# Optimization experiments

Measured on AMD Instinct MI355X. Metric: run time of the kernel, lower is better.

Reference implementation:

```python
import jax, jax.numpy as jnp
import numpy as np

N, E, H, NIN, DD = 10000, 160000, 128, 128, 256
SCALE = 30.0
EPS = 1e-5

def _ln(x, g, b):
    mu = jnp.mean(x, axis=-1, keepdims=True)
    var = jnp.mean((x - mu) ** 2, axis=-1, keepdims=True)
    return (x - mu) * jax.lax.rsqrt(var + EPS) * g + b

def _gelu(x):
    return jax.nn.gelu(x, approximate=False)  # torch nn.GELU default (erf)

def setup_inputs() -> dict:
    key = jax.random.key(0)
    ks = jax.random.split(key, 16)
    def w(k, i, o):
        return jax.random.normal(k, (i, o), jnp.float32) * (1.0 / np.sqrt(i))
    return {
        "h_V": jax.random.normal(ks[0], (N, H), jnp.float32),
        "h_E": jax.random.normal(ks[1], (E, H + NIN), jnp.float32),
        "edge_idx": jax.random.randint(ks[2], (2, E), 0, N, jnp.int32),
        # message MLP: (H+NIN)->H, H->H
        "m_w0": w(ks[3], H + NIN, H), "m_b0": jnp.zeros((H,), jnp.float32),
        "m_w1": w(ks[4], H, H),       "m_b1": jnp.zeros((H,), jnp.float32),
        # dense MLP: H->DD, DD->DD, final DD->H
        "d_w0": w(ks[5], H, DD),  "d_b0": jnp.zeros((DD,), jnp.float32),
        "d_w1": w(ks[6], DD, DD), "d_b1": jnp.zeros((DD,), jnp.float32),
        "d_w2": w(ks[7], DD, H),  "d_b2": jnp.zeros((H,), jnp.float32),
        # LayerNorm params
        "g1": jnp.ones((H,), jnp.float32), "be1": jnp.zeros((H,), jnp.float32),
        "g2": jnp.ones((H,), jnp.float32), "be2": jnp.zeros((H,), jnp.float32),
    }

def reference(h_V, h_E, edge_idx, m_w0, m_b0, m_w1, m_b1,
              d_w0, d_b0, d_w1, d_b1, d_w2, d_b2, g1, be1, g2, be2):
    src_idx = edge_idx[0]
    # message MLP over edges (dropout = identity at inference)
    h = _gelu(h_E @ m_w0 + m_b0)
    h_message = _gelu(h @ m_w1 + m_b1)          # [E, H]
    # scatter-sum aggregate edges -> nodes
    dh = jax.ops.segment_sum(h_message, src_idx, num_segments=N) / SCALE
    h_V = _ln(h_V + dh, g1, be1)
    # dense MLP over nodes
    d = _gelu(h_V @ d_w0 + d_b0)
    d = _gelu(d @ d_w1 + d_b1)
    dh = d @ d_w2 + d_b2
    return _ln(h_V + dh, g2, be2)
```

## Files before the change

kernel.cpp:

```cpp
#include <hip/hip_runtime.h>
#include <hip/hip_bf16.h>


typedef __attribute__((ext_vector_type(8))) short bf16x8;
typedef __attribute__((ext_vector_type(4))) float f32x4;

__device__ __forceinline__ unsigned short f2bf(float f) {
  union { float f; unsigned u; } v; v.f = f;
  return (unsigned short)((v.u + 0x7fffu + ((v.u >> 16) & 1u)) >> 16);
}
__device__ __forceinline__ unsigned pk2bf(float a, float b) {
  __hip_bfloat162 h = __float22bfloat162_rn(make_float2(a, b));
  union { __hip_bfloat162 h; unsigned u; } v; v.h = h;
  return v.u;
}
__device__ __forceinline__ float bf2f(unsigned s) {
  union { unsigned u; float f; } v; v.u = s << 16;
  return v.f;
}
__device__ __forceinline__ float gelu_f(float x) {
  float u = x * 0.70710678118654752f;
  float au = fabsf(u);
  float t = __builtin_amdgcn_rcpf(1.0f + 0.3275911f * au);
  float poly = ((((1.061405429f * t - 1.453152027f) * t + 1.421413741f) * t -
                 0.284496736f) * t + 0.254829592f) * t;
  float e = __expf(-au * au);
  float erfu = copysignf(1.0f - poly * e, u);
  return 0.5f * x * (1.0f + erfu);
}

__device__ __forceinline__ void gl2lds16(const void* g, void* l) {
  __builtin_amdgcn_global_load_lds((const __attribute__((address_space(1))) unsigned*)g,
                                   (__attribute__((address_space(3))) unsigned*)l, 16, 0, 0);
}

__global__ void k_pack(const float* __restrict__ mw0, const float* __restrict__ mw1,
                       const float* __restrict__ dw0, const float* __restrict__ dw1,
                       const float* __restrict__ dw2,
                       unsigned short* __restrict__ pw0, unsigned short* __restrict__ pw1,
                       unsigned short* __restrict__ pd0, unsigned short* __restrict__ pd1,
                       unsigned short* __restrict__ pd2) {
  int g = blockIdx.x, lane = threadIdx.x;
  const float* src; unsigned short* dst; int K, N, WC, base;
  if (g < 64)       { src = mw0; dst = pw0; K = 256; N = 128; WC = 32; base = 0; }
  else if (g < 96)  { src = mw1; dst = pw1; K = 128; N = 128; WC = 32; base = 64; }
  else if (g < 160) { src = dw0; dst = pd0; K = 128; N = 256; WC = 64; base = 96; }
  else if (g < 288) { src = dw1; dst = pd1; K = 256; N = 256; WC = 64; base = 160; }
  else              { src = dw2; dst = pd2; K = 256; N = 128; WC = 32; base = 288; }
  int lg = g - base;
  int KS = K >> 5, CTKS = (WC >> 4) * KS;
  int w = lg / CTKS, rem = lg % CTKS, ct = rem / KS, ks = rem % KS;
  int col = w * WC + ct * 16 + (lane & 15);
  int k0 = ks * 32 + (lane >> 4) * 8;
  unsigned short o[8];
#pragma unroll
  for (int j = 0; j < 8; ++j) o[j] = f2bf(src[(size_t)(k0 + j) * N + col]);
  uint4 u;
  u.x = (unsigned)o[0] | ((unsigned)o[1] << 16);
  u.y = (unsigned)o[2] | ((unsigned)o[3] << 16);
  u.z = (unsigned)o[4] | ((unsigned)o[5] << 16);
  u.w = (unsigned)o[6] | ((unsigned)o[7] << 16);
  *(uint4*)(dst + (size_t)(lg * 64 + lane) * 8) = u;
}

__global__ void k_hist(const int* __restrict__ eidx, int* __restrict__ counts, int E) {
  int e = blockIdx.x * 256 + threadIdx.x;
  if (e < E) atomicAdd(&counts[eidx[e]], 1);
}

__global__ __launch_bounds__(1024) void k_scan(const int* __restrict__ counts,
                                               int* __restrict__ row_start,
                                               int* __restrict__ cursor, int Nn) {
  __shared__ int sm[1024];
  int t = threadIdx.x;
  int chunk = (Nn + 1023) / 1024;
  int lo = t * chunk, hi = lo + chunk;
  if (hi > Nn) hi = Nn;
  int s = 0;
  for (int i = lo; i < hi; ++i) s += counts[i];
  sm[t] = s;
  __syncthreads();
  for (int o = 1; o < 1024; o <<= 1) {
    int u = (t >= o) ? sm[t - o] : 0;
    __syncthreads();
    sm[t] += u;
    __syncthreads();
  }
  int run = sm[t] - s;
  for (int i = lo; i < hi; ++i) {
    row_start[i] = run; cursor[i] = run; run += counts[i];
  }
  if (t == 1023) row_start[Nn] = sm[1023];
}

__global__ void k_scatter(const int* __restrict__ eidx, int* __restrict__ cursor,
                          int* __restrict__ eorder, int E) {
  int e = blockIdx.x * 256 + threadIdx.x;
  if (e < E) {
    int pos = atomicAdd(&cursor[eidx[e]], 1);
    eorder[pos] = e;
  }
}

#define AST 1040
#define ABUF 33280
__global__ __launch_bounds__(256, 2) void k_edge(
    const float* __restrict__ hE, const unsigned short* __restrict__ pw0,
    const unsigned short* __restrict__ pw1, const float* __restrict__ b0,
    const float* __restrict__ b1, unsigned short* __restrict__ hmsg, int E) {
  __shared__ __align__(16) char lds[2 * ABUF + 8192];
  char* Hb = lds + 2 * ABUF;
  const int tid = threadIdx.x;
  const int wid = tid >> 6, lane = tid & 63;
  const int l15 = lane & 15, lhi = lane >> 4;
  const int wcol = wid * 32;

  bf16x8 B0[16], B1[8];
  {
    const uint4* p0 = (const uint4*)pw0 + (size_t)(wid * 16) * 64 + lane;
#pragma unroll
    for (int f = 0; f < 16; ++f) { uint4 v = p0[(size_t)f * 64]; B0[f] = *(bf16x8*)&v; }
    const uint4* p1 = (const uint4*)pw1 + (size_t)(wid * 8) * 64 + lane;
#pragma unroll
    for (int f = 0; f < 8; ++f) { uint4 v = p1[(size_t)f * 64]; B1[f] = *(bf16x8*)&v; }
  }
  float bb0[2], bb1[2];
#pragma unroll
  for (int ct = 0; ct < 2; ++ct) {
    bb0[ct] = b0[wcol + ct * 16 + l15];
    bb1[ct] = b1[wcol + ct * 16 + l15];
  }
  __syncthreads();

  const int TILES = (E + 31) >> 5;
  auto STAGE = [&](int tile, int buf) {
    char* dstb = lds + buf * ABUF + (wid * 8) * AST;
#pragma unroll
    for (int i = 0; i < 8; ++i) {
      int grow = tile * 32 + wid * 8 + i;
      grow = grow < E ? grow : E - 1;
      const float* g = hE + (size_t)grow * 256 + lane * 4;
      gl2lds16(g, dstb + i * AST);
    }
  };

  int t = blockIdx.x;
  int cur = 0;
  if (t < TILES) STAGE(t, 0);
  for (; t < TILES; t += gridDim.x) {
    int tn = t + gridDim.x;
    if (tn < TILES) {
      STAGE(tn, cur ^ 1);
      asm volatile("s_waitcnt vmcnt(8)" ::: "memory");
    } else {
      asm volatile("s_waitcnt vmcnt(0)" ::: "memory");
    }
    __builtin_amdgcn_s_barrier();
    __builtin_amdgcn_sched_barrier(0);

    const char* A = lds + cur * ABUF;
    f32x4 acc[2][2];
#pragma unroll
    for (int mt = 0; mt < 2; ++mt)
#pragma unroll
      for (int ct = 0; ct < 2; ++ct) acc[mt][ct] = 0.f;
#pragma unroll
    for (int ks = 0; ks < 8; ++ks) {
      bf16x8 a[2];
#pragma unroll
      for (int mt = 0; mt < 2; ++mt) {
        int row = mt * 16 + l15;
        const char* p = A + row * AST + ks * 128 + lhi * 32;
        f32x4 lo = *(const f32x4*)p;
        f32x4 hi = *(const f32x4*)(p + 16);
        union { unsigned u[4]; bf16x8 v; } pk;
        pk.u[0] = pk2bf(lo[0], lo[1]);
        pk.u[1] = pk2bf(lo[2], lo[3]);
        pk.u[2] = pk2bf(hi[0], hi[1]);
        pk.u[3] = pk2bf(hi[2], hi[3]);
        a[mt] = pk.v;
      }
#pragma unroll
      for (int mt = 0; mt < 2; ++mt)
#pragma unroll
        for (int ct = 0; ct < 2; ++ct)
          acc[mt][ct] = __builtin_amdgcn_mfma_f32_16x16x32_bf16(a[mt], B0[ct * 8 + ks],
                                                               acc[mt][ct], 0, 0, 0);
    }
#pragma unroll
    for (int mt = 0; mt < 2; ++mt)
#pragma unroll
      for (int ct = 0; ct < 2; ++ct)
#pragma unroll
        for (int j = 0; j < 4; ++j) {
          int r = mt * 16 + lhi * 4 + j;
          int col = wcol + ct * 16 + l15;
          float g = gelu_f(acc[mt][ct][j] + bb0[ct]);
          *(unsigned short*)(Hb + r * 256 + ((col * 2) ^ ((r & 7) << 4))) = f2bf(g);
        }
    asm volatile("s_waitcnt lgkmcnt(0)" ::: "memory");
    __builtin_amdgcn_s_barrier();
    __builtin_amdgcn_sched_barrier(0);

    f32x4 acc2[2][2];
#pragma unroll
    for (int mt = 0; mt < 2; ++mt)
#pragma unroll
      for (int ct = 0; ct < 2; ++ct) acc2[mt][ct] = 0.f;
#pragma unroll
    for (int ks = 0; ks < 4; ++ks) {
      bf16x8 a[2];
#pragma unroll
      for (int mt = 0; mt < 2; ++mt) {
        int row = mt * 16 + l15;
        a[mt] = *(bf16x8*)(Hb + row * 256 + ((ks * 64 + lhi * 16) ^ ((row & 7) << 4)));
      }
#pragma unroll
      for (int mt = 0; mt < 2; ++mt)
#pragma unroll
        for (int ct = 0; ct < 2; ++ct)
          acc2[mt][ct] = __builtin_amdgcn_mfma_f32_16x16x32_bf16(a[mt], B1[ct * 4 + ks],
                                                                acc2[mt][ct], 0, 0, 0);
    }
    const int row0 = t * 32;
#pragma unroll
    for (int mt = 0; mt < 2; ++mt)
#pragma unroll
      for (int ct = 0; ct < 2; ++ct)
#pragma unroll
        for (int j = 0; j < 4; ++j) {
          int r = row0 + mt * 16 + lhi * 4 + j;
          if (r < E) {
            int col = wcol + ct * 16 + l15;
            hmsg[(size_t)r * 128 + col] = f2bf(gelu_f(acc2[mt][ct][j] + bb1[ct]));
          }
        }
    cur ^= 1;
  }
}

__global__ __launch_bounds__(256) void k_aggln(
    const unsigned* __restrict__ hmsg, const float2* __restrict__ hV,
    const int* __restrict__ row_start, const int* __restrict__ eorder,
    const float* __restrict__ g1, const float* __restrict__ be1,
    float2* __restrict__ hv1f, unsigned* __restrict__ hv1b, int Nn) {
  int wid = threadIdx.x >> 6, lane = threadIdx.x & 63;
  int node = blockIdx.x * 4 + wid;
  if (node >= Nn) return;
  int s = row_start[node], e = row_start[node + 1];
  float s0 = 0.f, s1 = 0.f;
  int i = s;
  for (; i + 3 < e; i += 4) {
    int e0 = eorder[i], e1 = eorder[i + 1], e2 = eorder[i + 2], e3 = eorder[i + 3];
    unsigned v0 = hmsg[(size_t)e0 * 64 + lane];
    unsigned v1 = hmsg[(size_t)e1 * 64 + lane];
    unsigned v2 = hmsg[(size_t)e2 * 64 + lane];
    unsigned v3 = hmsg[(size_t)e3 * 64 + lane];
    s0 += bf2f(v0 & 0xffffu) + bf2f(v1 & 0xffffu) + bf2f(v2 & 0xffffu) + bf2f(v3 & 0xffffu);
    s1 += bf2f(v0 >> 16) + bf2f(v1 >> 16) + bf2f(v2 >> 16) + bf2f(v3 >> 16);
  }
  for (; i < e; ++i) {
    unsigned v = hmsg[(size_t)eorder[i] * 64 + lane];
    s0 += bf2f(v & 0xffffu);
    s1 += bf2f(v >> 16);
  }
  float2 hv = hV[(size_t)node * 64 + lane];
  float x0 = hv.x + s0 * (1.f / 30.f);
  float x1 = hv.y + s1 * (1.f / 30.f);
  float sum = x0 + x1, sq = x0 * x0 + x1 * x1;
#pragma unroll
  for (int off = 32; off > 0; off >>= 1) {
    sum += __shfl_xor(sum, off);
    sq += __shfl_xor(sq, off);
  }
  float mu = sum * (1.f / 128.f);
  float var = sq * (1.f / 128.f) - mu * mu;
  float rs = rsqrtf(var + 1e-5f);
  int c = lane * 2;
  float y0 = (x0 - mu) * rs * g1[c] + be1[c];
  float y1 = (x1 - mu) * rs * g1[c + 1] + be1[c + 1];
  hv1f[(size_t)node * 64 + lane] = make_float2(y0, y1);
  hv1b[(size_t)node * 64 + lane] = (unsigned)f2bf(y0) | ((unsigned)f2bf(y1) << 16);
}

__global__ __launch_bounds__(256, 1) void k_node(
    const unsigned short* __restrict__ xb, const unsigned short* __restrict__ pd0,
    const unsigned short* __restrict__ pd1, const unsigned short* __restrict__ pd2,
    const float* __restrict__ db0, const float* __restrict__ db1,
    const float* __restrict__ db2, const float* __restrict__ hv1f,
    const float* __restrict__ g2, const float* __restrict__ be2,
    float* __restrict__ out, int Nn) {
  __shared__ __align__(16) char lds[16384 + 32768 + 32768];
  char* A0 = lds;
  char* D0 = lds + 16384;
  char* D1 = lds + 16384 + 32768;
  float* Y = (float*)D0;
  const int tid = threadIdx.x, wid = tid >> 6, lane = tid & 63;
  const int l15 = lane & 15, lhi = lane >> 4;
  const int row0 = blockIdx.x * 64;

#pragma unroll
  for (int p = 0; p < 4; ++p) {
    int idx = p * 256 + tid;
    int r = idx >> 4, c = idx & 15;
    uint4 v = make_uint4(0u, 0u, 0u, 0u);
    if (row0 + r < Nn) v = ((const uint4*)xb)[(size_t)(row0 + r) * 16 + c];
    *(uint4*)(A0 + r * 256 + ((c * 16) ^ ((r & 7) << 4))) = v;
  }
  __syncthreads();

  {
    f32x4 acc[4][4];
#pragma unroll
    for (int mt = 0; mt < 4; ++mt)
#pragma unroll
      for (int ct = 0; ct < 4; ++ct) acc[mt][ct] = 0.f;
#pragma unroll
    for (int ks = 0; ks < 4; ++ks) {
      bf16x8 a[4];
#pragma unroll
      for (int mt = 0; mt < 4; ++mt) {
        int row = mt * 16 + l15;
        a[mt] = *(bf16x8*)(A0 + row * 256 + ((ks * 64 + lhi * 16) ^ ((row & 7) << 4)));
      }
#pragma unroll
      for (int ct = 0; ct < 4; ++ct) {
        uint4 bv = ((const uint4*)pd0)[(size_t)(wid * 16 + ct * 4 + ks) * 64 + lane];
        bf16x8 b = *(bf16x8*)&bv;
#pragma unroll
        for (int mt = 0; mt < 4; ++mt)
          acc[mt][ct] = __builtin_amdgcn_mfma_f32_16x16x32_bf16(a[mt], b, acc[mt][ct], 0, 0, 0);
      }
    }
#pragma unroll
    for (int ct = 0; ct < 4; ++ct) {
      float bb = db0[wid * 64 + ct * 16 + l15];
      int col = wid * 64 + ct * 16 + l15;
#pragma unroll
      for (int mt = 0; mt < 4; ++mt)
#pragma unroll
        for (int j = 0; j < 4; ++j) {
          int r = mt * 16 + lhi * 4 + j;
          *(unsigned short*)(D0 + r * 512 + ((col * 2) ^ ((r & 7) << 4))) =
              f2bf(gelu_f(acc[mt][ct][j] + bb));
        }
    }
  }
  __syncthreads();

  {
    f32x4 acc[4][4];
#pragma unroll
    for (int mt = 0; mt < 4; ++mt)
#pragma unroll
      for (int ct = 0; ct < 4; ++ct) acc[mt][ct] = 0.f;
#pragma unroll
    for (int ks = 0; ks < 8; ++ks) {
      bf16x8 a[4];
#pragma unroll
      for (int mt = 0; mt < 4; ++mt) {
        int row = mt * 16 + l15;
        a[mt] = *(bf16x8*)(D0 + row * 512 + ((ks * 64 + lhi * 16) ^ ((row & 7) << 4)));
      }
#pragma unroll
      for (int ct = 0; ct < 4; ++ct) {
        uint4 bv = ((const uint4*)pd1)[(size_t)(wid * 32 + ct * 8 + ks) * 64 + lane];
        bf16x8 b = *(bf16x8*)&bv;
#pragma unroll
        for (int mt = 0; mt < 4; ++mt)
          acc[mt][ct] = __builtin_amdgcn_mfma_f32_16x16x32_bf16(a[mt], b, acc[mt][ct], 0, 0, 0);
      }
    }
#pragma unroll
    for (int ct = 0; ct < 4; ++ct) {
      float bb = db1[wid * 64 + ct * 16 + l15];
      int col = wid * 64 + ct * 16 + l15;
#pragma unroll
      for (int mt = 0; mt < 4; ++mt)
#pragma unroll
        for (int j = 0; j < 4; ++j) {
          int r = mt * 16 + lhi * 4 + j;
          *(unsigned short*)(D1 + r * 512 + ((col * 2) ^ ((r & 7) << 4))) =
              f2bf(gelu_f(acc[mt][ct][j] + bb));
        }
    }
  }
  __syncthreads();

  {
    f32x4 acc[4][2];
#pragma unroll
    for (int mt = 0; mt < 4; ++mt)
#pragma unroll
      for (int ct = 0; ct < 2; ++ct) acc[mt][ct] = 0.f;
#pragma unroll
    for (int ks = 0; ks < 8; ++ks) {
      bf16x8 a[4];
#pragma unroll
      for (int mt = 0; mt < 4; ++mt) {
        int row = mt * 16 + l15;
        a[mt] = *(bf16x8*)(D1 + row * 512 + ((ks * 64 + lhi * 16) ^ ((row & 7) << 4)));
      }
#pragma unroll
      for (int ct = 0; ct < 2; ++ct) {
        uint4 bv = ((const uint4*)pd2)[(size_t)(wid * 16 + ct * 8 + ks) * 64 + lane];
        bf16x8 b = *(bf16x8*)&bv;
#pragma unroll
        for (int mt = 0; mt < 4; ++mt)
          acc[mt][ct] = __builtin_amdgcn_mfma_f32_16x16x32_bf16(a[mt], b, acc[mt][ct], 0, 0, 0);
      }
    }
    __syncthreads();
#pragma unroll
    for (int ct = 0; ct < 2; ++ct) {
      float bb = db2[wid * 32 + ct * 16 + l15];
      int col = wid * 32 + ct * 16 + l15;
#pragma unroll
      for (int mt = 0; mt < 4; ++mt)
#pragma unroll
        for (int j = 0; j < 4; ++j) {
          int r = mt * 16 + lhi * 4 + j;
          int grow = row0 + r;
          float res = (grow < Nn) ? hv1f[(size_t)grow * 128 + col] : 0.f;
          Y[r * 128 + col] = acc[mt][ct][j] + bb + res;
        }
    }
  }
  __syncthreads();

  float g2a = g2[lane * 2], g2b = g2[lane * 2 + 1];
  float ba = be2[lane * 2], bbx = be2[lane * 2 + 1];
  for (int ii = 0; ii < 16; ++ii) {
    int r = wid * 16 + ii;
    int grow = row0 + r;
    if (grow >= Nn) continue;
    float2 xy = *(float2*)&Y[r * 128 + lane * 2];
    float sum = xy.x + xy.y, sq = xy.x * xy.x + xy.y * xy.y;
#pragma unroll
    for (int off = 32; off > 0; off >>= 1) {
      sum += __shfl_xor(sum, off);
      sq += __shfl_xor(sq, off);
    }
    float mu = sum * (1.f / 128.f);
    float var = sq * (1.f / 128.f) - mu * mu;
    float rs = rsqrtf(var + 1e-5f);
    float y0 = (xy.x - mu) * rs * g2a + ba;
    float y1 = (xy.y - mu) * rs * g2b + bbx;
    *(float2*)&out[(size_t)grow * 128 + lane * 2] = make_float2(y0, y1);
  }
}

extern "C" void kernel_launch(void* const* d_in, const int* in_sizes, int n_in,
                              void* d_out, int out_size, void* d_ws, size_t ws_size,
                              hipStream_t stream) {
  const float* hV  = (const float*)d_in[0];
  const float* hE  = (const float*)d_in[1];
  const int* eidx  = (const int*)d_in[2];
  const float* mw0 = (const float*)d_in[3];
  const float* mb0 = (const float*)d_in[4];
  const float* mw1 = (const float*)d_in[5];
  const float* mb1 = (const float*)d_in[6];
  const float* dw0 = (const float*)d_in[7];
  const float* db0 = (const float*)d_in[8];
  const float* dw1 = (const float*)d_in[9];
  const float* db1 = (const float*)d_in[10];
  const float* dw2 = (const float*)d_in[11];
  const float* db2 = (const float*)d_in[12];
  const float* g1  = (const float*)d_in[13];
  const float* be1 = (const float*)d_in[14];
  const float* g2  = (const float*)d_in[15];
  const float* be2 = (const float*)d_in[16];
  const int Nn = in_sizes[0] / 128;
  const int E  = in_sizes[1] / 256;

  char* ws = (char*)d_ws;
  size_t off = 0;
  auto alloc = [&](size_t bytes) -> char* {
    off = (off + 255) & ~(size_t)255;
    char* p = ws + off;
    off += bytes;
    return p;
  };
  unsigned short* hmsg = (unsigned short*)alloc((size_t)E * 128 * 2);
  float* hv1f          = (float*)alloc((size_t)Nn * 128 * 4);
  unsigned short* hv1b = (unsigned short*)alloc((size_t)Nn * 128 * 2);
  unsigned short* pw0  = (unsigned short*)alloc(32768 * 2);
  unsigned short* pw1  = (unsigned short*)alloc(16384 * 2);
  unsigned short* pd0  = (unsigned short*)alloc(32768 * 2);
  unsigned short* pd1  = (unsigned short*)alloc(65536 * 2);
  unsigned short* pd2  = (unsigned short*)alloc(32768 * 2);
  int* counts    = (int*)alloc((size_t)Nn * 4);
  int* row_start = (int*)alloc((size_t)(Nn + 1) * 4);
  int* cursor    = (int*)alloc((size_t)Nn * 4);
  int* eorder    = (int*)alloc((size_t)E * 4);

  hipMemsetAsync(counts, 0, (size_t)Nn * 4, stream);
  k_pack<<<352, 64, 0, stream>>>(mw0, mw1, dw0, dw1, dw2, pw0, pw1, pd0, pd1, pd2);
  k_hist<<<(E + 255) / 256, 256, 0, stream>>>(eidx, counts, E);
  k_scan<<<1, 1024, 0, stream>>>(counts, row_start, cursor, Nn);
  k_scatter<<<(E + 255) / 256, 256, 0, stream>>>(eidx, cursor, eorder, E);
  k_edge<<<512, 256, 0, stream>>>(hE, pw0, pw1, mb0, mb1, hmsg, E);
  k_aggln<<<(Nn + 3) / 4, 256, 0, stream>>>((const unsigned*)hmsg, (const float2*)hV,
                                            row_start, eorder, g1, be1,
                                            (float2*)hv1f, (unsigned*)hv1b, Nn);
  const int nt = (Nn + 63) / 64;
  k_node<<<nt, 256, 0, stream>>>(hv1b, pd0, pd1, pd2, db0, db1, db2,
                                 hv1f, g2, be2, (float*)d_out, Nn);
}
```

Measured before the change: 144.5 us.

## Stage edge inputs as bf16 via registers, coalesce message stores, raise occupancy

The edge kernel stops using async global-to-LDS fp32 copies. It prefetches the next tile's fp32 rows into registers, converts them to bf16 and writes them into a swizzled LDS buffer in the middle of the compute. This halves the LDS footprint, which allows three blocks per CU and a larger grid, and it takes the per-fragment conversion out of the MFMA loop. The output messages are staged through LDS and written as coalesced 16-byte stores. The counts memset is folded into the pack kernel to save a launch. The costs are extra register pressure from the prefetch and an additional barrier per tile.

```diff
diff --git a/kernel.cpp b/kernel.cpp
--- a/kernel.cpp
+++ b/kernel.cpp
@@ -29,18 +29,16 @@
   return 0.5f * x * (1.0f + erfu);
 }
 
-__device__ __forceinline__ void gl2lds16(const void* g, void* l) {
-  __builtin_amdgcn_global_load_lds((const __attribute__((address_space(1))) unsigned*)g,
-                                   (__attribute__((address_space(3))) unsigned*)l, 16, 0, 0);
-}
-
 __global__ void k_pack(const float* __restrict__ mw0, const float* __restrict__ mw1,
                        const float* __restrict__ dw0, const float* __restrict__ dw1,
                        const float* __restrict__ dw2,
                        unsigned short* __restrict__ pw0, unsigned short* __restrict__ pw1,
                        unsigned short* __restrict__ pd0, unsigned short* __restrict__ pd1,
-                       unsigned short* __restrict__ pd2) {
+                       unsigned short* __restrict__ pd2,
+                       int* __restrict__ counts, int Nn) {
   int g = blockIdx.x, lane = threadIdx.x;
+  int z = g * 64 + lane;
+  if (z < Nn) counts[z] = 0;
   const float* src; unsigned short* dst; int K, N, WC, base;
   if (g < 64)       { src = mw0; dst = pw0; K = 256; N = 128; WC = 32; base = 0; }
   else if (g < 96)  { src = mw1; dst = pw1; K = 128; N = 128; WC = 32; base = 64; }
@@ -102,14 +100,12 @@
   }
 }
 
-#define AST 1040
-#define ABUF 33280
-__global__ __launch_bounds__(256, 2) void k_edge(
+__global__ __launch_bounds__(256, 3) void k_edge(
     const float* __restrict__ hE, const unsigned short* __restrict__ pw0,
     const unsigned short* __restrict__ pw1, const float* __restrict__ b0,
     const float* __restrict__ b1, unsigned short* __restrict__ hmsg, int E) {
-  __shared__ __align__(16) char lds[2 * ABUF + 8192];
-  char* Hb = lds + 2 * ABUF;
+  __shared__ __align__(16) char lds[2 * 16384 + 8192];
+  char* Hb = lds + 32768;
   const int tid = threadIdx.x;
   const int wid = tid >> 6, lane = tid & 63;
   const int l15 = lane & 15, lhi = lane >> 4;
@@ -130,35 +126,40 @@
     bb0[ct] = b0[wcol + ct * 16 + l15];
     bb1[ct] = b1[wcol + ct * 16 + l15];
   }
-  __syncthreads();
 
   const int TILES = (E + 31) >> 5;
-  auto STAGE = [&](int tile, int buf) {
-    char* dstb = lds + buf * ABUF + (wid * 8) * AST;
-#pragma unroll
-    for (int i = 0; i < 8; ++i) {
-      int grow = tile * 32 + wid * 8 + i;
-      grow = grow < E ? grow : E - 1;
-      const float* g = hE + (size_t)grow * 256 + lane * 4;
-      gl2lds16(g, dstb + i * AST);
-    }
-  };
-
   int t = blockIdx.x;
+  if (t >= TILES) return;
+
+  {
+#pragma unroll
+    for (int p = 0; p < 8; ++p) {
+      int idx = p * 256 + tid;
+      int r = idx >> 6, c4 = idx & 63;
+      int grow = t * 32 + r; grow = grow < E ? grow : E - 1;
+      float4 v = ((const float4*)hE)[(size_t)grow * 64 + c4];
+      uint2 u; u.x = pk2bf(v.x, v.y); u.y = pk2bf(v.z, v.w);
+      *(uint2*)(lds + r * 512 + ((c4 * 8) ^ ((r & 7) << 4))) = u;
+    }
+    __syncthreads();
+  }
+
   int cur = 0;
-  if (t < TILES) STAGE(t, 0);
   for (; t < TILES; t += gridDim.x) {
-    int tn = t + gridDim.x;
+    const int tn = t + gridDim.x;
+    const int row0 = t * 32;
+    float4 lv[8];
     if (tn < TILES) {
-      STAGE(tn, cur ^ 1);
-      asm volatile("s_waitcnt vmcnt(8)" ::: "memory");
-    } else {
-      asm volatile("s_waitcnt vmcnt(0)" ::: "memory");
-    }
-    __builtin_amdgcn_s_barrier();
-    __builtin_amdgcn_sched_barrier(0);
-
-    const char* A = lds + cur * ABUF;
+#pragma unroll
+      for (int p = 0; p < 8; ++p) {
+        int idx = p * 256 + tid;
+        int r = idx >> 6, c4 = idx & 63;
+        int grow = tn * 32 + r; grow = grow < E ? grow : E - 1;
+        lv[p] = ((const float4*)hE)[(size_t)grow * 64 + c4];
+      }
+    }
+
+    const char* A = lds + cur * 16384;
     f32x4 acc[2][2];
 #pragma unroll
     for (int mt = 0; mt < 2; ++mt)
@@ -170,15 +171,7 @@
 #pragma unroll
       for (int mt = 0; mt < 2; ++mt) {
         int row = mt * 16 + l15;
-        const char* p = A + row * AST + ks * 128 + lhi * 32;
-        f32x4 lo = *(const f32x4*)p;
-        f32x4 hi = *(const f32x4*)(p + 16);
-        union { unsigned u[4]; bf16x8 v; } pk;
-        pk.u[0] = pk2bf(lo[0], lo[1]);
-        pk.u[1] = pk2bf(lo[2], lo[3]);
-        pk.u[2] = pk2bf(hi[0], hi[1]);
-        pk.u[3] = pk2bf(hi[2], hi[3]);
-        a[mt] = pk.v;
+        a[mt] = *(bf16x8*)(A + row * 512 + ((ks * 64 + lhi * 16) ^ ((row & 7) << 4)));
       }
 #pragma unroll
       for (int mt = 0; mt < 2; ++mt)
@@ -198,9 +191,18 @@
           float g = gelu_f(acc[mt][ct][j] + bb0[ct]);
           *(unsigned short*)(Hb + r * 256 + ((col * 2) ^ ((r & 7) << 4))) = f2bf(g);
         }
-    asm volatile("s_waitcnt lgkmcnt(0)" ::: "memory");
-    __builtin_amdgcn_s_barrier();
-    __builtin_amdgcn_sched_barrier(0);
+    __syncthreads();
+
+    if (tn < TILES) {
+      char* Anx = lds + (cur ^ 1) * 16384;
+#pragma unroll
+      for (int p = 0; p < 8; ++p) {
+        int idx = p * 256 + tid;
+        int r = idx >> 6, c4 = idx & 63;
+        uint2 u; u.x = pk2bf(lv[p].x, lv[p].y); u.y = pk2bf(lv[p].z, lv[p].w);
+        *(uint2*)(Anx + r * 512 + ((c4 * 8) ^ ((r & 7) << 4))) = u;
+      }
+    }
 
     f32x4 acc2[2][2];
 #pragma unroll
@@ -222,19 +224,31 @@
           acc2[mt][ct] = __builtin_amdgcn_mfma_f32_16x16x32_bf16(a[mt], B1[ct * 4 + ks],
                                                                 acc2[mt][ct], 0, 0, 0);
     }
-    const int row0 = t * 32;
+    char* Acur = lds + cur * 16384;
 #pragma unroll
     for (int mt = 0; mt < 2; ++mt)
 #pragma unroll
       for (int ct = 0; ct < 2; ++ct)
 #pragma unroll
         for (int j = 0; j < 4; ++j) {
-          int r = row0 + mt * 16 + lhi * 4 + j;
-          if (r < E) {
-            int col = wcol + ct * 16 + l15;
-            hmsg[(size_t)r * 128 + col] = f2bf(gelu_f(acc2[mt][ct][j] + bb1[ct]));
-          }
+          int r = mt * 16 + lhi * 4 + j;
+          int col = wcol + ct * 16 + l15;
+          float g = gelu_f(acc2[mt][ct][j] + bb1[ct]);
+          *(unsigned short*)(Acur + r * 256 + ((col * 2) ^ ((r & 7) << 4))) = f2bf(g);
         }
+    __syncthreads();
+
+    {
+      int r = tid >> 3;
+      int base = (tid & 7) * 32;
+      uint4 c0 = *(uint4*)(Acur + r * 256 + (base ^ ((r & 7) << 4)));
+      uint4 c1 = *(uint4*)(Acur + r * 256 + ((base + 16) ^ ((r & 7) << 4)));
+      int grow = row0 + r;
+      if (grow < E) {
+        uint4* dst = (uint4*)(hmsg + (size_t)grow * 128) + (tid & 7) * 2;
+        dst[0] = c0; dst[1] = c1;
+      }
+    }
     cur ^= 1;
   }
 }
@@ -494,12 +508,12 @@
   int* cursor    = (int*)alloc((size_t)Nn * 4);
   int* eorder    = (int*)alloc((size_t)E * 4);
 
-  hipMemsetAsync(counts, 0, (size_t)Nn * 4, stream);
-  k_pack<<<352, 64, 0, stream>>>(mw0, mw1, dw0, dw1, dw2, pw0, pw1, pd0, pd1, pd2);
+  k_pack<<<352, 64, 0, stream>>>(mw0, mw1, dw0, dw1, dw2, pw0, pw1, pd0, pd1, pd2,
+                                 counts, Nn);
   k_hist<<<(E + 255) / 256, 256, 0, stream>>>(eidx, counts, E);
   k_scan<<<1, 1024, 0, stream>>>(counts, row_start, cursor, Nn);
   k_scatter<<<(E + 255) / 256, 256, 0, stream>>>(eidx, cursor, eorder, E);
-  k_edge<<<512, 256, 0, stream>>>(hE, pw0, pw1, mb0, mb1, hmsg, E);
+  k_edge<<<768, 256, 0, stream>>>(hE, pw0, pw1, mb0, mb1, hmsg, E);
   k_aggln<<<(Nn + 3) / 4, 256, 0, stream>>>((const unsigned*)hmsg, (const float2*)hV,
                                             row_start, eorder, g1, be1,
                                             (float2*)hv1f, (unsigned*)hv1b, Nn);
```

Result: slower. 212.0 us (+46.7%).
